# Kernel tuning notes

Hardware: AMD Instinct MI355X
Metric: run time of the kernel (lower is better)

## Reference

```python
import jax, jax.numpy as jnp
import numpy as np

INPUT_SIZE = 512
HIDDEN_SIZE = 1024
OUTPUT_SIZE = 512
BATCH = 128
SEQ_LEN = 512


def setup_inputs() -> dict:
    key = jax.random.key(0)
    k_x, k_xh, k_hh, k_yh = jax.random.split(key, 4)

    def xavier(k, shape):
        fan_in, fan_out = shape
        lim = float(np.sqrt(6.0 / (fan_in + fan_out)))
        return jax.random.uniform(k, shape, jnp.float32, -lim, lim)

    return {
        "x": jax.random.normal(k_x, (BATCH, SEQ_LEN, INPUT_SIZE), jnp.float32),
        "W_xh": xavier(k_xh, (INPUT_SIZE, HIDDEN_SIZE)),
        "W_hh": xavier(k_hh, (HIDDEN_SIZE, HIDDEN_SIZE)),
        "W_yh": xavier(k_yh, (HIDDEN_SIZE, OUTPUT_SIZE)),
        "W_bh": jnp.zeros((HIDDEN_SIZE,), jnp.float32),
        "W_by": jnp.zeros((OUTPUT_SIZE,), jnp.float32),
    }


def reference(x, W_xh, W_hh, W_yh, W_bh, W_by):
    # x: [B, S, I]. Precompute input projections for all steps (parallel GEMM),
    # then scan the strictly sequential hidden recurrence.
    xW = jnp.einsum("bsi,ih->bsh", x, W_xh) + W_bh  # [B, S, H]
    h0 = jnp.zeros((x.shape[0], W_hh.shape[0]), x.dtype)

    def step(h, xw_t):
        h_new = jnp.tanh(xw_t + h @ W_hh)
        return h_new, None

    h_last, _ = jax.lax.scan(step, h0, jnp.swapaxes(xW, 0, 1))  # scan over S
    return h_last @ W_yh + W_by  # [B, O]
```

## Files before the change

### kernel.cpp

```cpp
#include <hip/hip_runtime.h>

typedef _Float16 half8 __attribute__((ext_vector_type(8)));
typedef float f32x4 __attribute__((ext_vector_type(4)));
typedef unsigned long long u64;

#define MFMA16(a,b,c) __builtin_amdgcn_mfma_f32_16x16x32_f16((a),(b),(c),0,0,0)

constexpr int B_SZ = 128, S_LEN = 512, I_SZ = 512, H_SZ = 1024, O_SZ = 512;

constexpr size_t XW_OFF   = 0;
constexpr size_t X16_OFF  = XW_OFF   + (size_t)S_LEN * B_SZ * H_SZ * 2;
constexpr size_t WXHT_OFF = X16_OFF  + (size_t)B_SZ * S_LEN * I_SZ * 2;
constexpr size_t WHHT_OFF = WXHT_OFF + (size_t)H_SZ * I_SZ * 2;
constexpr size_t WYHT_OFF = WHHT_OFF + (size_t)H_SZ * I_SZ * 2 + (size_t)H_SZ * H_SZ * 2 - (size_t)H_SZ * I_SZ * 2;
constexpr size_t HB_OFF   = WYHT_OFF + (size_t)O_SZ * H_SZ * 2;
constexpr size_t TAG_OFF  = HB_OFF   + (size_t)8 * 2 * 16 * 1024 * 2;

__device__ __forceinline__ u64 ag_load64(const u64* p) {
  return __hip_atomic_load(p, __ATOMIC_RELAXED, __HIP_MEMORY_SCOPE_AGENT);
}
__device__ __forceinline__ unsigned ag_load32(const unsigned* p) {
  return __hip_atomic_load(p, __ATOMIC_RELAXED, __HIP_MEMORY_SCOPE_AGENT);
}
__device__ __forceinline__ void ag_store32(unsigned* p, unsigned v) {
  __hip_atomic_store(p, v, __ATOMIC_RELAXED, __HIP_MEMORY_SCOPE_AGENT);
}
__device__ __forceinline__ void ag_xchg64(u64* p, u64 v) {
  (void)__hip_atomic_exchange(p, v, __ATOMIC_RELAXED, __HIP_MEMORY_SCOPE_AGENT);
}

__device__ __forceinline__ float ftanh(float z) {
  float e = __builtin_amdgcn_exp2f(z * 2.8853900817779268f);
  return fmaf(-2.f, __builtin_amdgcn_rcpf(e + 1.f), 1.f);
}

__global__ void k_cvt_x(const float* __restrict__ in, _Float16* __restrict__ out) {
  size_t i = ((size_t)blockIdx.x * 256 + threadIdx.x) * 8;
  float4 a = *(const float4*)(in + i);
  float4 b = *(const float4*)(in + i + 4);
  half8 h;
  h[0] = (_Float16)a.x; h[1] = (_Float16)a.y; h[2] = (_Float16)a.z; h[3] = (_Float16)a.w;
  h[4] = (_Float16)b.x; h[5] = (_Float16)b.y; h[6] = (_Float16)b.z; h[7] = (_Float16)b.w;
  *(half8*)(out + i) = h;
}

__global__ void k_transpose_cvt(const float* __restrict__ in, _Float16* __restrict__ out,
                                int K, int N) {
  int k = blockIdx.x * 256 + threadIdx.x;
  int n = blockIdx.y;
  out[(size_t)n * K + k] = (_Float16)in[(size_t)k * N + n];
}

__launch_bounds__(256, 1)
__global__ void k_xw_gemm(const _Float16* __restrict__ A,
                          const _Float16* __restrict__ BT,
                          const float* __restrict__ bias,
                          _Float16* __restrict__ xw)
{
  const int m0 = blockIdx.y * 128;
  const int n0 = blockIdx.x * 128;
  __shared__ __align__(16) _Float16 la[128][72];
  __shared__ __align__(16) _Float16 lb[128][72];
  const int tid = threadIdx.x;
  const int w = tid >> 6, l = tid & 63;
  const int wr = w >> 1, wc = w & 1;
  const int cl = l & 15;
  const int kh = (l >> 4) << 3;
  const int rl = (l >> 4) << 2;

  f32x4 acc[4][4] = {};

  for (int kb = 0; kb < 512; kb += 64) {
    {
      const int r = tid >> 1, sg = tid & 1;
      const _Float16* ga = A  + (size_t)(m0 + r) * 512 + kb + sg * 32;
      const _Float16* gb = BT + (size_t)(n0 + r) * 512 + kb + sg * 32;
      _Float16* da = &la[r][sg * 32];
      _Float16* db = &lb[r][sg * 32];
      #pragma unroll
      for (int i = 0; i < 4; i++) *(half8*)(da + i * 8) = *(const half8*)(ga + i * 8);
      #pragma unroll
      for (int i = 0; i < 4; i++) *(half8*)(db + i * 8) = *(const half8*)(gb + i * 8);
    }
    __syncthreads();
    #pragma unroll
    for (int kk = 0; kk < 64; kk += 32) {
      half8 af[4], bf[4];
      #pragma unroll
      for (int mi = 0; mi < 4; mi++) af[mi] = *(const half8*)(&la[wr * 64 + mi * 16 + cl][kk + kh]);
      #pragma unroll
      for (int ni = 0; ni < 4; ni++) bf[ni] = *(const half8*)(&lb[wc * 64 + ni * 16 + cl][kk + kh]);
      #pragma unroll
      for (int mi = 0; mi < 4; mi++)
        #pragma unroll
        for (int ni = 0; ni < 4; ni++)
          acc[mi][ni] = MFMA16(af[mi], bf[ni], acc[mi][ni]);
    }
    __syncthreads();
  }

  #pragma unroll
  for (int mi = 0; mi < 4; mi++)
    #pragma unroll
    for (int ni = 0; ni < 4; ni++) {
      const int col = n0 + wc * 64 + ni * 16 + cl;
      const float bv = bias[col];
      #pragma unroll
      for (int r = 0; r < 4; r++) {
        const int m = m0 + wr * 64 + mi * 16 + rl + r;
        const int b = m >> 9;
        const int s = m & 511;
        xw[((size_t)(s * B_SZ + b) << 10) + col] = (_Float16)(acc[mi][ni][r] + bv);
      }
    }
}


__device__ __forceinline__ void poll_tags64(const unsigned* gtag, int l, unsigned t) {
  for (int it = 0; it < (1 << 17); ++it) {
    unsigned tg = ag_load32(gtag + l);
    if (__all((int)(tg >= t))) break;
    __builtin_amdgcn_s_sleep(1);
  }
  __builtin_amdgcn_sched_barrier(0);
}

__launch_bounds__(128, 1)
__global__ void k_rnn(const _Float16* __restrict__ xw,
                      const _Float16* __restrict__ WhhT,
                      const _Float16* __restrict__ WyhT,
                      const float* __restrict__ Wby,
                      u64* __restrict__ hb,
                      unsigned* __restrict__ tags,
                      float* __restrict__ out)
{
  __shared__ __align__(16) _Float16 lw[32][1032];
  __shared__ __align__(16) _Float16 lh[2][16][1032];
  __shared__ __align__(16) _Float16 st[2][16][40];

  const int bid = blockIdx.x;
  const int g = bid & 7, j = bid >> 3;
  const int tid = threadIdx.x;
  const int w = tid >> 6, l = tid & 63;
  const int cl = l & 15;
  const int kh = (l >> 4) << 3;
  const int rl = (l >> 4) << 2;
  const int r0 = g << 4;
  const int n0 = j << 5;
  const int colg = n0 + (w << 4) + cl;
  const int hr = tid >> 3, hs = tid & 7;
  unsigned* gtag = tags + (g << 6);
  const int slot = (j << 1) + w;
  u64* hbg = hb + ((size_t)g << 13);

  {
    const int rr = tid >> 2, sg = tid & 3;
    const _Float16* src = WhhT + ((size_t)(n0 + rr) << 10) + (sg << 8);
    _Float16* dst = &lw[rr][sg << 8];
    #pragma unroll
    for (int i = 0; i < 32; i++)
      *(half8*)(dst + (i << 3)) = *(const half8*)(src + (i << 3));
  }
  __syncthreads();

  for (int t = 0; t < 512; t++) {
    float xv[4];
    {
      const _Float16* p = xw + ((size_t)(t * 128 + r0 + rl) << 10) + colg;
      #pragma unroll
      for (int r = 0; r < 4; r++) xv[r] = (float)p[(size_t)r << 10];
    }

    if (t > 0) {
      poll_tags64(gtag, l, (unsigned)t);
      u64 a[32];
      const u64* hsrc = hbg + ((size_t)(t & 1) << 12) + (hr << 8) + (hs << 1);
      #pragma unroll
      for (int i = 0; i < 16; i++) {
        a[2 * i]     = ag_load64(hsrc + (i << 4));
        a[2 * i + 1] = ag_load64(hsrc + (i << 4) + 1);
      }
      _Float16* ld = &lh[t & 1][hr][hs << 3];
      #pragma unroll
      for (int i = 0; i < 16; i++) {
        *(u64*)(ld + (i << 6))     = a[2 * i];
        *(u64*)(ld + (i << 6) + 4) = a[2 * i + 1];
      }
    }
    __syncthreads();

    f32x4 acc0 = {}, acc1 = {};
    if (t > 0) {
      const _Float16 (*lhb)[1032] = lh[t & 1];
      #pragma unroll 4
      for (int kc = 0; kc < 32; kc += 2) {
        half8 a0 = *(const half8*)&lhb[cl][(kc << 5) + kh];
        half8 b0 = *(const half8*)&lw[(w << 4) + cl][(kc << 5) + kh];
        acc0 = MFMA16(a0, b0, acc0);
        half8 a1 = *(const half8*)&lhb[cl][((kc + 1) << 5) + kh];
        half8 b1 = *(const half8*)&lw[(w << 4) + cl][((kc + 1) << 5) + kh];
        acc1 = MFMA16(a1, b1, acc1);
      }
    }

    #pragma unroll
    for (int r = 0; r < 4; r++) {
      float z = xv[r] + acc0[r] + acc1[r];
      st[w][rl + r][cl] = (_Float16)ftanh(z);
    }
    asm volatile("s_waitcnt lgkmcnt(0)" ::: "memory");
    __builtin_amdgcn_sched_barrier(0);
    {
      u64 pv = *(const u64*)&st[w][l >> 2][(l & 3) << 2];
      u64* dst = hbg + ((size_t)((t + 1) & 1) << 12) + ((size_t)(l >> 2) << 8)
               + (j << 3) + (w << 2) + (l & 3);
      ag_xchg64(dst, pv);
    }
    asm volatile("s_waitcnt vmcnt(0)" ::: "memory");
    if (l == 0) ag_store32(gtag + slot, (unsigned)(t + 1));
  }

  poll_tags64(gtag, l, 512u);
  {
    u64 a[32];
    const u64* hsrc = hbg + (hr << 8) + (hs << 1);
    #pragma unroll
    for (int i = 0; i < 16; i++) {
      a[2 * i]     = ag_load64(hsrc + (i << 4));
      a[2 * i + 1] = ag_load64(hsrc + (i << 4) + 1);
    }
    _Float16* ld = &lh[0][hr][hs << 3];
    #pragma unroll
    for (int i = 0; i < 16; i++) {
      *(u64*)(ld + (i << 6))     = a[2 * i];
      *(u64*)(ld + (i << 6) + 4) = a[2 * i + 1];
    }
  }
  __syncthreads();
  if (w == 0) {
    f32x4 a0 = {}, a1 = {};
    const int oc = (j << 4) + cl;
    const _Float16* bsrc = WyhT + ((size_t)oc << 10);
    #pragma unroll 4
    for (int kc = 0; kc < 32; kc += 2) {
      half8 av  = *(const half8*)&lh[0][cl][(kc << 5) + kh];
      half8 bv  = *(const half8*)(bsrc + (kc << 5) + kh);
      a0 = MFMA16(av, bv, a0);
      half8 av1 = *(const half8*)&lh[0][cl][((kc + 1) << 5) + kh];
      half8 bv1 = *(const half8*)(bsrc + ((kc + 1) << 5) + kh);
      a1 = MFMA16(av1, bv1, a1);
    }
    const float bb = Wby[oc];
    #pragma unroll
    for (int r = 0; r < 4; r++)
      out[((size_t)(r0 + rl + r) << 9) + oc] = a0[r] + a1[r] + bb;
  }
}

extern "C" void kernel_launch(void* const* d_in, const int* in_sizes, int n_in,
                              void* d_out, int out_size, void* d_ws, size_t ws_size,
                              hipStream_t stream) {
  const float* x   = (const float*)d_in[0];
  const float* Wxh = (const float*)d_in[1];
  const float* Whh = (const float*)d_in[2];
  const float* Wyh = (const float*)d_in[3];
  const float* Wbh = (const float*)d_in[4];
  const float* Wby = (const float*)d_in[5];
  float* out = (float*)d_out;

  char* ws = (char*)d_ws;
  _Float16* xw   = (_Float16*)(ws + XW_OFF);
  _Float16* x16  = (_Float16*)(ws + X16_OFF);
  _Float16* WxhT = (_Float16*)(ws + WXHT_OFF);
  _Float16* WhhT = (_Float16*)(ws + WHHT_OFF);
  _Float16* WyhT = (_Float16*)(ws + WYHT_OFF);
  u64*      hb   = (u64*)(ws + HB_OFF);
  unsigned* tags = (unsigned*)(ws + TAG_OFF);

  hipMemsetAsync(tags, 0, 8 * 64 * sizeof(unsigned), stream);

  k_cvt_x<<<16384, 256, 0, stream>>>(x, x16);
  k_transpose_cvt<<<dim3(2, 1024), 256, 0, stream>>>(Wxh, WxhT, 512, 1024);
  k_transpose_cvt<<<dim3(4, 1024), 256, 0, stream>>>(Whh, WhhT, 1024, 1024);
  k_transpose_cvt<<<dim3(4, 512),  256, 0, stream>>>(Wyh, WyhT, 1024, 512);

  k_xw_gemm<<<dim3(8, 512), 256, 0, stream>>>(x16, WxhT, Wbh, xw);

  k_rnn<<<256, 128, 0, stream>>>(xw, WhhT, WyhT, Wby, hb, tags, out);
}
```

Before: 2.055 ms.

## Fuse epoch tags into hidden-state words and poll data directly in a single-wave RNN

Each 64-bit hidden-state word now carries the fp16 data in its high half and the step epoch in its low half. Consumers poll the data words themselves instead of a separate tag array, which removes the writer's store-fence-tag sequence and the reader's tag-then-data round trip. Each block now runs as one wave that computes both 16-column tiles. It feeds the polled registers straight into MFMA, with no LDS staging or __syncthreads, and overlaps the polling of later k-chunks with MFMA on earlier ones. In exchange, memory traffic per step doubles because of the epoch bits. The tag memset is also gone, so epochs left in the workspace by a previous call could be mistaken for fresh data on later runs.

```diff
diff --git a/kernel.cpp b/kernel.cpp
--- a/kernel.cpp
+++ b/kernel.cpp
@@ -2,6 +2,7 @@
 
 typedef _Float16 half8 __attribute__((ext_vector_type(8)));
 typedef float f32x4 __attribute__((ext_vector_type(4)));
+typedef unsigned uint32x4 __attribute__((ext_vector_type(4)));
 typedef unsigned long long u64;
 
 #define MFMA16(a,b,c) __builtin_amdgcn_mfma_f32_16x16x32_f16((a),(b),(c),0,0,0)
@@ -12,21 +13,18 @@
 constexpr size_t X16_OFF  = XW_OFF   + (size_t)S_LEN * B_SZ * H_SZ * 2;
 constexpr size_t WXHT_OFF = X16_OFF  + (size_t)B_SZ * S_LEN * I_SZ * 2;
 constexpr size_t WHHT_OFF = WXHT_OFF + (size_t)H_SZ * I_SZ * 2;
-constexpr size_t WYHT_OFF = WHHT_OFF + (size_t)H_SZ * I_SZ * 2 + (size_t)H_SZ * H_SZ * 2 - (size_t)H_SZ * I_SZ * 2;
+constexpr size_t WYHT_OFF = WHHT_OFF + (size_t)H_SZ * H_SZ * 2;
 constexpr size_t HB_OFF   = WYHT_OFF + (size_t)O_SZ * H_SZ * 2;
-constexpr size_t TAG_OFF  = HB_OFF   + (size_t)8 * 2 * 16 * 1024 * 2;
+
+constexpr size_t HB_ROW   = 512;
+constexpr size_t HB_PAR   = 16 * HB_ROW;
+constexpr size_t HB_GRP   = 2 * HB_PAR;
 
 __device__ __forceinline__ u64 ag_load64(const u64* p) {
   return __hip_atomic_load(p, __ATOMIC_RELAXED, __HIP_MEMORY_SCOPE_AGENT);
 }
-__device__ __forceinline__ unsigned ag_load32(const unsigned* p) {
-  return __hip_atomic_load(p, __ATOMIC_RELAXED, __HIP_MEMORY_SCOPE_AGENT);
-}
-__device__ __forceinline__ void ag_store32(unsigned* p, unsigned v) {
+__device__ __forceinline__ void ag_store64(u64* p, u64 v) {
   __hip_atomic_store(p, v, __ATOMIC_RELAXED, __HIP_MEMORY_SCOPE_AGENT);
-}
-__device__ __forceinline__ void ag_xchg64(u64* p, u64 v) {
-  (void)__hip_atomic_exchange(p, v, __ATOMIC_RELAXED, __HIP_MEMORY_SCOPE_AGENT);
 }
 
 __device__ __forceinline__ float ftanh(float z) {
@@ -116,144 +114,178 @@
 }
 
 
-__device__ __forceinline__ void poll_tags64(const unsigned* gtag, int l, unsigned t) {
-  for (int it = 0; it < (1 << 17); ++it) {
-    unsigned tg = ag_load32(gtag + l);
-    if (__all((int)(tg >= t))) break;
+template<int BLK0>
+__device__ __forceinline__ void issueq(u64 (&buf)[8][4], const u64* hrow) {
+  #pragma unroll
+  for (int b = 0; b < 8; b++)
+    #pragma unroll
+    for (int k = 0; k < 4; k++)
+      buf[b][k] = ag_load64(hrow + ((BLK0 + b) << 4) + k);
+}
+
+template<int BLK0>
+__device__ __forceinline__ unsigned epbad(const u64 (&buf)[8][4], unsigned ep) {
+  unsigned bad = 0;
+  #pragma unroll
+  for (int b = 0; b < 8; b++)
+    #pragma unroll
+    for (int k = 0; k < 4; k++)
+      bad |= ((unsigned)buf[b][k]) ^ ep;
+  return bad;
+}
+
+template<int BLK0>
+__device__ __forceinline__ void checkq(u64 (&buf)[8][4], const u64* hrow, unsigned ep) {
+  unsigned bad = epbad<BLK0>(buf, ep);
+  for (int it = 0; bad && it < (1 << 12); ++it) {
     __builtin_amdgcn_s_sleep(1);
-  }
-  __builtin_amdgcn_sched_barrier(0);
-}
-
-__launch_bounds__(128, 1)
+    issueq<BLK0>(buf, hrow);
+    bad = epbad<BLK0>(buf, ep);
+  }
+}
+
+template<int BLK0>
+__device__ __forceinline__ void pollq(u64 (&buf)[8][4], const u64* hrow, unsigned ep) {
+  issueq<BLK0>(buf, hrow);
+  checkq<BLK0>(buf, hrow, ep);
+}
+
+template<int BLK0>
+__device__ __forceinline__ void mfmaq(const u64 (&buf)[8][4],
+                                      const _Float16 (*lw)[1032],
+                                      int cl, int kh, f32x4 (&acc)[2][2]) {
+  #pragma unroll
+  for (int b = 0; b < 8; b++) {
+    uint32x4 u;
+    #pragma unroll
+    for (int k = 0; k < 4; k++) u[k] = (unsigned)(buf[b][k] >> 32);
+    half8 a = __builtin_bit_cast(half8, u);
+    const int p = BLK0 + b;
+    half8 w0 = *(const half8*)&lw[cl][(p << 5) + kh];
+    half8 w1 = *(const half8*)&lw[16 + cl][(p << 5) + kh];
+    acc[0][p & 1] = MFMA16(a, w0, acc[0][p & 1]);
+    acc[1][p & 1] = MFMA16(a, w1, acc[1][p & 1]);
+  }
+}
+
+template<int BLK0>
+__device__ __forceinline__ void mfmaq_o(const u64 (&buf)[8][4],
+                                        const _Float16* bsrc,
+                                        int kh, f32x4 (&oa)[2]) {
+  #pragma unroll
+  for (int b = 0; b < 8; b++) {
+    uint32x4 u;
+    #pragma unroll
+    for (int k = 0; k < 4; k++) u[k] = (unsigned)(buf[b][k] >> 32);
+    half8 a = __builtin_bit_cast(half8, u);
+    const int p = BLK0 + b;
+    half8 wv = *(const half8*)(bsrc + (p << 5) + kh);
+    oa[p & 1] = MFMA16(a, wv, oa[p & 1]);
+  }
+}
+
+__launch_bounds__(64, 1)
 __global__ void k_rnn(const _Float16* __restrict__ xw,
                       const _Float16* __restrict__ WhhT,
                       const _Float16* __restrict__ WyhT,
                       const float* __restrict__ Wby,
                       u64* __restrict__ hb,
-                      unsigned* __restrict__ tags,
                       float* __restrict__ out)
 {
   __shared__ __align__(16) _Float16 lw[32][1032];
-  __shared__ __align__(16) _Float16 lh[2][16][1032];
-  __shared__ __align__(16) _Float16 st[2][16][40];
+  __shared__ __align__(16) _Float16 stb[16][40];
 
   const int bid = blockIdx.x;
   const int g = bid & 7, j = bid >> 3;
-  const int tid = threadIdx.x;
-  const int w = tid >> 6, l = tid & 63;
-  const int cl = l & 15;
-  const int kh = (l >> 4) << 3;
-  const int rl = (l >> 4) << 2;
-  const int r0 = g << 4;
-  const int n0 = j << 5;
-  const int colg = n0 + (w << 4) + cl;
-  const int hr = tid >> 3, hs = tid & 7;
-  unsigned* gtag = tags + (g << 6);
-  const int slot = (j << 1) + w;
-  u64* hbg = hb + ((size_t)g << 13);
-
-  {
-    const int rr = tid >> 2, sg = tid & 3;
-    const _Float16* src = WhhT + ((size_t)(n0 + rr) << 10) + (sg << 8);
-    _Float16* dst = &lw[rr][sg << 8];
-    #pragma unroll
-    for (int i = 0; i < 32; i++)
-      *(half8*)(dst + (i << 3)) = *(const half8*)(src + (i << 3));
-  }
-  __syncthreads();
+  const int l = threadIdx.x;
+  const int cl  = l & 15;
+  const int kh  = (l >> 4) << 3;
+  const int kh4 = (l >> 4) << 2;
+  const int rl  = (l >> 4) << 2;
+  const int r0  = g << 4;
+  const int n0  = j << 5;
+  u64* hbg = hb + (size_t)g * HB_GRP;
+
+  for (int i = l; i < 32 * 128; i += 64) {
+    const int row = i >> 7, c8 = (i & 127) << 3;
+    *(half8*)&lw[row][c8] = *(const half8*)&WhhT[((size_t)(n0 + row) << 10) + c8];
+  }
 
   for (int t = 0; t < 512; t++) {
-    float xv[4];
+    float xv[2][4];
     {
-      const _Float16* p = xw + ((size_t)(t * 128 + r0 + rl) << 10) + colg;
-      #pragma unroll
-      for (int r = 0; r < 4; r++) xv[r] = (float)p[(size_t)r << 10];
-    }
-
+      const _Float16* p = xw + ((size_t)(t * 128 + r0 + rl) << 10) + n0 + cl;
+      #pragma unroll
+      for (int f = 0; f < 2; f++)
+        #pragma unroll
+        for (int r = 0; r < 4; r++)
+          xv[f][r] = (float)p[((size_t)r << 10) + (f << 4)];
+    }
+
+    f32x4 acc[2][2] = {{{}, {}}, {{}, {}}};
     if (t > 0) {
-      poll_tags64(gtag, l, (unsigned)t);
-      u64 a[32];
-      const u64* hsrc = hbg + ((size_t)(t & 1) << 12) + (hr << 8) + (hs << 1);
-      #pragma unroll
-      for (int i = 0; i < 16; i++) {
-        a[2 * i]     = ag_load64(hsrc + (i << 4));
-        a[2 * i + 1] = ag_load64(hsrc + (i << 4) + 1);
+      const unsigned ep = (unsigned)t;
+      const u64* hrow = hbg + (size_t)(t & 1) * HB_PAR + (size_t)cl * HB_ROW + kh4;
+      u64 qa[8][4], qb[8][4];
+      pollq<0>(qa, hrow, ep);
+      issueq<8>(qb, hrow);
+      mfmaq<0>(qa, lw, cl, kh, acc);
+      checkq<8>(qb, hrow, ep);
+      issueq<16>(qa, hrow);
+      mfmaq<8>(qb, lw, cl, kh, acc);
+      checkq<16>(qa, hrow, ep);
+      issueq<24>(qb, hrow);
+      mfmaq<16>(qa, lw, cl, kh, acc);
+      checkq<24>(qb, hrow, ep);
+      mfmaq<24>(qb, lw, cl, kh, acc);
+    }
+
+    #pragma unroll
+    for (int f = 0; f < 2; f++)
+      #pragma unroll
+      for (int r = 0; r < 4; r++) {
+        float z = xv[f][r] + acc[f][0][r] + acc[f][1][r];
+        stb[rl + r][(f << 4) + cl] = (_Float16)ftanh(z);
       }
-      _Float16* ld = &lh[t & 1][hr][hs << 3];
-      #pragma unroll
-      for (int i = 0; i < 16; i++) {
-        *(u64*)(ld + (i << 6))     = a[2 * i];
-        *(u64*)(ld + (i << 6) + 4) = a[2 * i + 1];
-      }
-    }
-    __syncthreads();
-
-    f32x4 acc0 = {}, acc1 = {};
-    if (t > 0) {
-      const _Float16 (*lhb)[1032] = lh[t & 1];
-      #pragma unroll 4
-      for (int kc = 0; kc < 32; kc += 2) {
-        half8 a0 = *(const half8*)&lhb[cl][(kc << 5) + kh];
-        half8 b0 = *(const half8*)&lw[(w << 4) + cl][(kc << 5) + kh];
-        acc0 = MFMA16(a0, b0, acc0);
-        half8 a1 = *(const half8*)&lhb[cl][((kc + 1) << 5) + kh];
-        half8 b1 = *(const half8*)&lw[(w << 4) + cl][((kc + 1) << 5) + kh];
-        acc1 = MFMA16(a1, b1, acc1);
-      }
-    }
-
-    #pragma unroll
-    for (int r = 0; r < 4; r++) {
-      float z = xv[r] + acc0[r] + acc1[r];
-      st[w][rl + r][cl] = (_Float16)ftanh(z);
-    }
     asm volatile("s_waitcnt lgkmcnt(0)" ::: "memory");
     __builtin_amdgcn_sched_barrier(0);
     {
-      u64 pv = *(const u64*)&st[w][l >> 2][(l & 3) << 2];
-      u64* dst = hbg + ((size_t)((t + 1) & 1) << 12) + ((size_t)(l >> 2) << 8)
-               + (j << 3) + (w << 2) + (l & 3);
-      ag_xchg64(dst, pv);
-    }
-    asm volatile("s_waitcnt vmcnt(0)" ::: "memory");
-    if (l == 0) ag_store32(gtag + slot, (unsigned)(t + 1));
-  }
-
-  poll_tags64(gtag, l, 512u);
+      const int row = l >> 2, c4 = (l & 3) << 2;
+      const unsigned* sp = (const unsigned*)&stb[row][(l & 3) << 3];
+      unsigned d[4];
+      #pragma unroll
+      for (int k = 0; k < 4; k++) d[k] = sp[k];
+      u64* dst = hbg + (size_t)((t + 1) & 1) * HB_PAR + (size_t)row * HB_ROW + (j << 4) + c4;
+      const u64 epn = (u64)(unsigned)(t + 1);
+      #pragma unroll
+      for (int k = 0; k < 4; k++)
+        ag_store64(dst + k, ((u64)d[k] << 32) | epn);
+    }
+  }
+
   {
-    u64 a[32];
-    const u64* hsrc = hbg + (hr << 8) + (hs << 1);
-    #pragma unroll
-    for (int i = 0; i < 16; i++) {
-      a[2 * i]     = ag_load64(hsrc + (i << 4));
-      a[2 * i + 1] = ag_load64(hsrc + (i << 4) + 1);
-    }
-    _Float16* ld = &lh[0][hr][hs << 3];
-    #pragma unroll
-    for (int i = 0; i < 16; i++) {
-      *(u64*)(ld + (i << 6))     = a[2 * i];
-      *(u64*)(ld + (i << 6) + 4) = a[2 * i + 1];
-    }
-  }
-  __syncthreads();
-  if (w == 0) {
-    f32x4 a0 = {}, a1 = {};
+    const unsigned ep = 512u;
+    const u64* hrow = hbg + (size_t)cl * HB_ROW + kh4;
     const int oc = (j << 4) + cl;
     const _Float16* bsrc = WyhT + ((size_t)oc << 10);
-    #pragma unroll 4
-    for (int kc = 0; kc < 32; kc += 2) {
-      half8 av  = *(const half8*)&lh[0][cl][(kc << 5) + kh];
-      half8 bv  = *(const half8*)(bsrc + (kc << 5) + kh);
-      a0 = MFMA16(av, bv, a0);
-      half8 av1 = *(const half8*)&lh[0][cl][((kc + 1) << 5) + kh];
-      half8 bv1 = *(const half8*)(bsrc + ((kc + 1) << 5) + kh);
-      a1 = MFMA16(av1, bv1, a1);
-    }
+    f32x4 oa[2] = {{}, {}};
+    u64 qa[8][4], qb[8][4];
+    pollq<0>(qa, hrow, ep);
+    issueq<8>(qb, hrow);
+    mfmaq_o<0>(qa, bsrc, kh, oa);
+    checkq<8>(qb, hrow, ep);
+    issueq<16>(qa, hrow);
+    mfmaq_o<8>(qb, bsrc, kh, oa);
+    checkq<16>(qa, hrow, ep);
+    issueq<24>(qb, hrow);
+    mfmaq_o<16>(qa, bsrc, kh, oa);
+    checkq<24>(qb, hrow, ep);
+    mfmaq_o<24>(qb, bsrc, kh, oa);
+
     const float bb = Wby[oc];
     #pragma unroll
     for (int r = 0; r < 4; r++)
-      out[((size_t)(r0 + rl + r) << 9) + oc] = a0[r] + a1[r] + bb;
+      out[((size_t)(r0 + rl + r) << 9) + oc] = oa[0][r] + oa[1][r] + bb;
   }
 }
 
@@ -275,9 +307,6 @@
   _Float16* WhhT = (_Float16*)(ws + WHHT_OFF);
   _Float16* WyhT = (_Float16*)(ws + WYHT_OFF);
   u64*      hb   = (u64*)(ws + HB_OFF);
-  unsigned* tags = (unsigned*)(ws + TAG_OFF);
-
-  hipMemsetAsync(tags, 0, 8 * 64 * sizeof(unsigned), stream);
 
   k_cvt_x<<<16384, 256, 0, stream>>>(x, x16);
   k_transpose_cvt<<<dim3(2, 1024), 256, 0, stream>>>(Wxh, WxhT, 512, 1024);
@@ -286,5 +315,5 @@
 
   k_xw_gemm<<<dim3(8, 512), 256, 0, stream>>>(x16, WxhT, Wbh, xw);
 
-  k_rnn<<<256, 128, 0, stream>>>(xw, WhhT, WyhT, Wby, hb, tags, out);
-}
+  k_rnn<<<256, 64, 0, stream>>>(xw, WhhT, WyhT, Wby, hb, out);
+}
```

Measured after the change: 3.161 ms. +53.8%, slower.

## Halve RNN workgroups, widen per-wave columns, stream h directly into MFMA registers

Applied to the files above, without the earlier changes.

The persistent recurrent kernel now runs 128 workgroups instead of 256. Each wave computes 32 hidden columns, so each group of 16 workgroups shares 32 tags instead of 64. The hidden state is stored in an MFMA-fragment-friendly layout and loaded from global memory straight into registers in pipelined chunks, interleaved with MFMAs. This removes the LDS staging round-trip and one __syncthreads per step. The intent is to cut per-step synchronization and latency on the sequential critical path, at the cost of twice the MFMA work per wave and more LDS for weights.

```diff
diff --git a/kernel.cpp b/kernel.cpp
--- a/kernel.cpp
+++ b/kernel.cpp
@@ -3,6 +3,7 @@
 typedef _Float16 half8 __attribute__((ext_vector_type(8)));
 typedef float f32x4 __attribute__((ext_vector_type(4)));
 typedef unsigned long long u64;
+typedef u64 u64x2 __attribute__((ext_vector_type(2)));
 
 #define MFMA16(a,b,c) __builtin_amdgcn_mfma_f32_16x16x32_f16((a),(b),(c),0,0,0)
 
@@ -12,21 +13,21 @@
 constexpr size_t X16_OFF  = XW_OFF   + (size_t)S_LEN * B_SZ * H_SZ * 2;
 constexpr size_t WXHT_OFF = X16_OFF  + (size_t)B_SZ * S_LEN * I_SZ * 2;
 constexpr size_t WHHT_OFF = WXHT_OFF + (size_t)H_SZ * I_SZ * 2;
-constexpr size_t WYHT_OFF = WHHT_OFF + (size_t)H_SZ * I_SZ * 2 + (size_t)H_SZ * H_SZ * 2 - (size_t)H_SZ * I_SZ * 2;
+constexpr size_t WYHT_OFF = WHHT_OFF + (size_t)H_SZ * H_SZ * 2;
 constexpr size_t HB_OFF   = WYHT_OFF + (size_t)O_SZ * H_SZ * 2;
-constexpr size_t TAG_OFF  = HB_OFF   + (size_t)8 * 2 * 16 * 1024 * 2;
+constexpr size_t TAG_OFF  = HB_OFF   + (size_t)8 * 8192 * 8;
 
 __device__ __forceinline__ u64 ag_load64(const u64* p) {
   return __hip_atomic_load(p, __ATOMIC_RELAXED, __HIP_MEMORY_SCOPE_AGENT);
 }
+__device__ __forceinline__ void ag_store64(u64* p, u64 v) {
+  __hip_atomic_store(p, v, __ATOMIC_RELAXED, __HIP_MEMORY_SCOPE_AGENT);
+}
 __device__ __forceinline__ unsigned ag_load32(const unsigned* p) {
   return __hip_atomic_load(p, __ATOMIC_RELAXED, __HIP_MEMORY_SCOPE_AGENT);
 }
 __device__ __forceinline__ void ag_store32(unsigned* p, unsigned v) {
   __hip_atomic_store(p, v, __ATOMIC_RELAXED, __HIP_MEMORY_SCOPE_AGENT);
-}
-__device__ __forceinline__ void ag_xchg64(u64* p, u64 v) {
-  (void)__hip_atomic_exchange(p, v, __ATOMIC_RELAXED, __HIP_MEMORY_SCOPE_AGENT);
 }
 
 __device__ __forceinline__ float ftanh(float z) {
@@ -116,13 +117,52 @@
 }
 
 
-__device__ __forceinline__ void poll_tags64(const unsigned* gtag, int l, unsigned t) {
+__device__ __forceinline__ void poll_tags(const unsigned* gtag, int l, unsigned t) {
   for (int it = 0; it < (1 << 17); ++it) {
-    unsigned tg = ag_load32(gtag + l);
+    unsigned tg = ag_load32(gtag + (l & 31));
     if (__all((int)(tg >= t))) break;
     __builtin_amdgcn_s_sleep(1);
   }
   __builtin_amdgcn_sched_barrier(0);
+}
+
+template<int BLK0>
+__device__ __forceinline__ void issueq8(u64 (&buf)[8][2], const u64* hrow) {
+  #pragma unroll
+  for (int b = 0; b < 8; b++) {
+    buf[b][0] = ag_load64(hrow + ((BLK0 + b) << 7));
+    buf[b][1] = ag_load64(hrow + ((BLK0 + b) << 7) + 1);
+  }
+}
+
+template<int BLK0>
+__device__ __forceinline__ void mfmaq8(const u64 (&buf)[8][2],
+                                       const _Float16 (*lw)[1032],
+                                       int w, int cl, int kh, f32x4 (&acc)[2][2]) {
+  #pragma unroll
+  for (int b = 0; b < 8; b++) {
+    const int p = BLK0 + b;
+    u64x2 w2 = { buf[b][0], buf[b][1] };
+    half8 a = __builtin_bit_cast(half8, w2);
+    half8 b0 = *(const half8*)&lw[(w << 5) + cl][(p << 5) + kh];
+    half8 b1 = *(const half8*)&lw[(w << 5) + 16 + cl][(p << 5) + kh];
+    acc[0][p & 1] = MFMA16(a, b0, acc[0][p & 1]);
+    acc[1][p & 1] = MFMA16(a, b1, acc[1][p & 1]);
+  }
+}
+
+template<int BLK0>
+__device__ __forceinline__ void mfmaq_o8(const u64 (&buf)[8][2],
+                                         const _Float16* bsrc,
+                                         int kh, f32x4 (&oa)[2]) {
+  #pragma unroll
+  for (int b = 0; b < 8; b++) {
+    const int p = BLK0 + b;
+    u64x2 w2 = { buf[b][0], buf[b][1] };
+    half8 a = __builtin_bit_cast(half8, w2);
+    half8 bv = *(const half8*)(bsrc + (p << 5) + kh);
+    oa[p & 1] = MFMA16(a, bv, oa[p & 1]);
+  }
 }
 
 __launch_bounds__(128, 1)
@@ -134,126 +174,96 @@
                       unsigned* __restrict__ tags,
                       float* __restrict__ out)
 {
-  __shared__ __align__(16) _Float16 lw[32][1032];
-  __shared__ __align__(16) _Float16 lh[2][16][1032];
-  __shared__ __align__(16) _Float16 st[2][16][40];
+  __shared__ __align__(16) _Float16 lw[64][1032];
+  __shared__ __align__(16) _Float16 stb[2][16][40];
 
   const int bid = blockIdx.x;
   const int g = bid & 7, j = bid >> 3;
   const int tid = threadIdx.x;
   const int w = tid >> 6, l = tid & 63;
-  const int cl = l & 15;
-  const int kh = (l >> 4) << 3;
-  const int rl = (l >> 4) << 2;
-  const int r0 = g << 4;
-  const int n0 = j << 5;
-  const int colg = n0 + (w << 4) + cl;
-  const int hr = tid >> 3, hs = tid & 7;
-  unsigned* gtag = tags + (g << 6);
-  const int slot = (j << 1) + w;
+  const int p_self = (j << 1) | w;
+  const int cl  = l & 15;
+  const int kh  = (l >> 4) << 3;
+  const int kh2 = (l >> 4) << 1;
+  const int rl  = (l >> 4) << 2;
+  const int r0  = g << 4;
+  const int colbase = p_self << 5;
+  unsigned* gtag = tags + (g << 5);
   u64* hbg = hb + ((size_t)g << 13);
 
-  {
-    const int rr = tid >> 2, sg = tid & 3;
-    const _Float16* src = WhhT + ((size_t)(n0 + rr) << 10) + (sg << 8);
-    _Float16* dst = &lw[rr][sg << 8];
+  for (int i = tid; i < 64 * 128; i += 128) {
+    const int row = i >> 7, c8 = (i & 127) << 3;
+    *(half8*)&lw[row][c8] = *(const half8*)&WhhT[((size_t)((j << 6) + row) << 10) + c8];
+  }
+  __syncthreads();
+
+  for (int t = 0; t < 512; t++) {
+    float xv[2][4];
+    {
+      const _Float16* p = xw + ((size_t)(t * 128 + r0 + rl) << 10) + colbase + cl;
+      #pragma unroll
+      for (int f = 0; f < 2; f++)
+        #pragma unroll
+        for (int r = 0; r < 4; r++)
+          xv[f][r] = (float)p[((size_t)r << 10) + (f << 4)];
+    }
+
+    f32x4 acc[2][2] = {{{}, {}}, {{}, {}}};
+    if (t > 0) {
+      poll_tags(gtag, l, (unsigned)t);
+      const u64* hrow = hbg + ((size_t)(t & 1) << 12) + (cl << 3) + kh2;
+      u64 qa[8][2], qb[8][2];
+      issueq8<0>(qa, hrow);
+      issueq8<8>(qb, hrow);
+      mfmaq8<0>(qa, lw, w, cl, kh, acc);
+      issueq8<16>(qa, hrow);
+      mfmaq8<8>(qb, lw, w, cl, kh, acc);
+      issueq8<24>(qb, hrow);
+      mfmaq8<16>(qa, lw, w, cl, kh, acc);
+      mfmaq8<24>(qb, lw, w, cl, kh, acc);
+    }
+
     #pragma unroll
-    for (int i = 0; i < 32; i++)
-      *(half8*)(dst + (i << 3)) = *(const half8*)(src + (i << 3));
-  }
-  __syncthreads();
-
-  for (int t = 0; t < 512; t++) {
-    float xv[4];
-    {
-      const _Float16* p = xw + ((size_t)(t * 128 + r0 + rl) << 10) + colg;
-      #pragma unroll
-      for (int r = 0; r < 4; r++) xv[r] = (float)p[(size_t)r << 10];
-    }
-
-    if (t > 0) {
-      poll_tags64(gtag, l, (unsigned)t);
-      u64 a[32];
-      const u64* hsrc = hbg + ((size_t)(t & 1) << 12) + (hr << 8) + (hs << 1);
-      #pragma unroll
-      for (int i = 0; i < 16; i++) {
-        a[2 * i]     = ag_load64(hsrc + (i << 4));
-        a[2 * i + 1] = ag_load64(hsrc + (i << 4) + 1);
+    for (int f = 0; f < 2; f++)
+      #pragma unroll
+      for (int r = 0; r < 4; r++) {
+        float z = xv[f][r] + acc[f][0][r] + acc[f][1][r];
+        stb[w][rl + r][(f << 4) + cl] = (_Float16)ftanh(z);
       }
-      _Float16* ld = &lh[t & 1][hr][hs << 3];
-      #pragma unroll
-      for (int i = 0; i < 16; i++) {
-        *(u64*)(ld + (i << 6))     = a[2 * i];
-        *(u64*)(ld + (i << 6) + 4) = a[2 * i + 1];
-      }
-    }
-    __syncthreads();
-
-    f32x4 acc0 = {}, acc1 = {};
-    if (t > 0) {
-      const _Float16 (*lhb)[1032] = lh[t & 1];
-      #pragma unroll 4
-      for (int kc = 0; kc < 32; kc += 2) {
-        half8 a0 = *(const half8*)&lhb[cl][(kc << 5) + kh];
-        half8 b0 = *(const half8*)&lw[(w << 4) + cl][(kc << 5) + kh];
-        acc0 = MFMA16(a0, b0, acc0);
-        half8 a1 = *(const half8*)&lhb[cl][((kc + 1) << 5) + kh];
-        half8 b1 = *(const half8*)&lw[(w << 4) + cl][((kc + 1) << 5) + kh];
-        acc1 = MFMA16(a1, b1, acc1);
-      }
-    }
-
-    #pragma unroll
-    for (int r = 0; r < 4; r++) {
-      float z = xv[r] + acc0[r] + acc1[r];
-      st[w][rl + r][cl] = (_Float16)ftanh(z);
-    }
     asm volatile("s_waitcnt lgkmcnt(0)" ::: "memory");
     __builtin_amdgcn_sched_barrier(0);
     {
-      u64 pv = *(const u64*)&st[w][l >> 2][(l & 3) << 2];
-      u64* dst = hbg + ((size_t)((t + 1) & 1) << 12) + ((size_t)(l >> 2) << 8)
-               + (j << 3) + (w << 2) + (l & 3);
-      ag_xchg64(dst, pv);
+      const u64* sp = (const u64*)&stb[w][l >> 2][(l & 3) << 3];
+      u64 p0 = sp[0], p1 = sp[1];
+      u64* dst = hbg + ((size_t)((t + 1) & 1) << 12) + (p_self << 7)
+               + ((l >> 2) << 3) + ((l & 3) << 1);
+      ag_store64(dst, p0);
+      ag_store64(dst + 1, p1);
     }
     asm volatile("s_waitcnt vmcnt(0)" ::: "memory");
-    if (l == 0) ag_store32(gtag + slot, (unsigned)(t + 1));
-  }
-
-  poll_tags64(gtag, l, 512u);
+    if (l == 0) ag_store32(gtag + p_self, (unsigned)(t + 1));
+  }
+
+  poll_tags(gtag, l, 512u);
   {
-    u64 a[32];
-    const u64* hsrc = hbg + (hr << 8) + (hs << 1);
-    #pragma unroll
-    for (int i = 0; i < 16; i++) {
-      a[2 * i]     = ag_load64(hsrc + (i << 4));
-      a[2 * i + 1] = ag_load64(hsrc + (i << 4) + 1);
-    }
-    _Float16* ld = &lh[0][hr][hs << 3];
-    #pragma unroll
-    for (int i = 0; i < 16; i++) {
-      *(u64*)(ld + (i << 6))     = a[2 * i];
-      *(u64*)(ld + (i << 6) + 4) = a[2 * i + 1];
-    }
-  }
-  __syncthreads();
-  if (w == 0) {
-    f32x4 a0 = {}, a1 = {};
-    const int oc = (j << 4) + cl;
+    const u64* hrow = hbg + (cl << 3) + kh2;
+    const int oc = (p_self << 4) + cl;
     const _Float16* bsrc = WyhT + ((size_t)oc << 10);
-    #pragma unroll 4
-    for (int kc = 0; kc < 32; kc += 2) {
-      half8 av  = *(const half8*)&lh[0][cl][(kc << 5) + kh];
-      half8 bv  = *(const half8*)(bsrc + (kc << 5) + kh);
-      a0 = MFMA16(av, bv, a0);
-      half8 av1 = *(const half8*)&lh[0][cl][((kc + 1) << 5) + kh];
-      half8 bv1 = *(const half8*)(bsrc + ((kc + 1) << 5) + kh);
-      a1 = MFMA16(av1, bv1, a1);
-    }
+    f32x4 oa[2] = {{}, {}};
+    u64 qa[8][2], qb[8][2];
+    issueq8<0>(qa, hrow);
+    issueq8<8>(qb, hrow);
+    mfmaq_o8<0>(qa, bsrc, kh, oa);
+    issueq8<16>(qa, hrow);
+    mfmaq_o8<8>(qb, bsrc, kh, oa);
+    issueq8<24>(qb, hrow);
+    mfmaq_o8<16>(qa, bsrc, kh, oa);
+    mfmaq_o8<24>(qb, bsrc, kh, oa);
+
     const float bb = Wby[oc];
     #pragma unroll
     for (int r = 0; r < 4; r++)
-      out[((size_t)(r0 + rl + r) << 9) + oc] = a0[r] + a1[r] + bb;
+      out[((size_t)(r0 + rl + r) << 9) + oc] = oa[0][r] + oa[1][r] + bb;
   }
 }
 
@@ -277,7 +287,7 @@
   u64*      hb   = (u64*)(ws + HB_OFF);
   unsigned* tags = (unsigned*)(ws + TAG_OFF);
 
-  hipMemsetAsync(tags, 0, 8 * 64 * sizeof(unsigned), stream);
+  hipMemsetAsync(tags, 0, 8 * 32 * sizeof(unsigned), stream);
 
   k_cvt_x<<<16384, 256, 0, stream>>>(x, x16);
   k_transpose_cvt<<<dim3(2, 1024), 256, 0, stream>>>(Wxh, WxhT, 512, 1024);
@@ -286,5 +296,5 @@
 
   k_xw_gemm<<<dim3(8, 512), 256, 0, stream>>>(x16, WxhT, Wbh, xw);
 
-  k_rnn<<<256, 128, 0, stream>>>(xw, WhhT, WyhT, Wby, hb, tags, out);
-}
+  k_rnn<<<128, 128, 0, stream>>>(xw, WhhT, WyhT, Wby, hb, tags, out);
+}
```

New measurement: 1.977 ms. -3.8%, faster.
